# Kernel optimization log

Hardware: AMD Instinct MI355X
Metric: run time of the kernel (lower is better)

The kernel has to match this reference:

```python
import jax, jax.numpy as jnp
import numpy as np

# Module hyperparameters (init_kwargs)
NUM_EXPERTS = 8
HIDDEN = 1024
CAP_FACTORS = [0.5, 0.75, 1.0, 1.0, 1.25, 1.25, 1.5, 1.5]


def setup_inputs() -> dict:
    key = jax.random.key(0)
    k1, k2, k3 = jax.random.split(key, 3)
    G, T = 4, 2048
    token_inputs = jax.random.normal(k1, (G, T, HIDDEN), dtype=jnp.float32)
    # RouterWeights = nn.Linear(hidden, num_experts, bias=True)
    W = jax.random.normal(k2, (HIDDEN, NUM_EXPERTS), dtype=jnp.float32) * (1.0 / np.sqrt(HIDDEN))
    b = jax.random.normal(k3, (NUM_EXPERTS,), dtype=jnp.float32) * 0.01
    return {"token_inputs": token_inputs, "W": W, "b": b, "expert_capacity": 256}


def reference(token_inputs, W, b, expert_capacity):
    # token_inputs: [G, T, H]; jitter_noise=0 so no jitter; ignore_padding_tokens=False
    G, T, _ = token_inputs.shape
    logits = jnp.einsum("gth,he->gte", token_inputs, W) + b  # [G, T, E]
    probs = jax.nn.softmax(logits, axis=-1)
    # router z-loss: mean(logsumexp(logits, -1)^2)
    z_loss = jnp.mean(jax.nn.logsumexp(logits, axis=-1) ** 2)

    capacities = [int(expert_capacity * f) for f in CAP_FACTORS]
    max_cap = max(capacities)

    dispatch_slices = []  # each [G, T, max_cap] int32
    combine_slices = []   # each [G, T, max_cap] float32
    for e, cap in enumerate(capacities):
        gate, idx = jax.lax.top_k(probs[:, :, e], cap)  # [G, cap]
        # one_hot(idx, T): [G, cap, T] -> transpose to [G, T, cap]
        oh = jax.nn.one_hot(idx, T, dtype=jnp.int32).transpose(0, 2, 1)  # [G, T, cap]
        oh = jnp.pad(oh, ((0, 0), (0, 0), (0, max_cap - cap)))
        dispatch_slices.append(oh)
        # combine: gate broadcast over tokens dim (as in original code)
        comb = jnp.broadcast_to(gate[:, None, :], (G, T, cap))  # [G, T, cap]
        comb = jnp.pad(comb, ((0, 0), (0, 0), (0, max_cap - cap)))
        combine_slices.append(comb)

    dispatch_mask = jnp.stack(dispatch_slices, axis=1)  # [G, E, T, max_cap]
    combine_array = jnp.stack(combine_slices, axis=1).astype(jnp.float32)  # [G, E, T, max_cap]
    auxiliary_loss = jnp.float32(0.0)
    return dispatch_mask, combine_array, auxiliary_loss, z_loss
```

## Files before the change

kernel.cpp:

```cpp
#include <hip/hip_runtime.h>
#include <hip/hip_bf16.h>
#include <math.h>

#define G 4
#define T 2048
#define H 1024
#define E 8
#define NSORT (G * E)

typedef float f4 __attribute__((ext_vector_type(4)));

__global__ __launch_bounds__(256) void router_logits(
    const float* __restrict__ x, const float* __restrict__ W,
    const float* __restrict__ b, float* __restrict__ probs,
    float* __restrict__ lse2) {
  int wave = (int)((blockIdx.x * blockDim.x + threadIdx.x) >> 6);
  int lane = threadIdx.x & 63;
  if (wave >= G * T) return;
  const float* xr = x + (size_t)wave * H;

  double acc0 = 0, acc1 = 0, acc2 = 0, acc3 = 0;
  double acc4 = 0, acc5 = 0, acc6 = 0, acc7 = 0;
#pragma unroll
  for (int j = 0; j < 4; ++j) {
    int hbase = j * 256 + lane * 4;
    f4 xv = *(const f4*)(xr + hbase);
#pragma unroll
    for (int k = 0; k < 4; ++k) {
      const float* wr = W + (size_t)(hbase + k) * 8;
      f4 w0 = *(const f4*)(wr);
      f4 w1 = *(const f4*)(wr + 4);
      double xd = (double)xv[k];
      acc0 += xd * (double)w0[0];
      acc1 += xd * (double)w0[1];
      acc2 += xd * (double)w0[2];
      acc3 += xd * (double)w0[3];
      acc4 += xd * (double)w1[0];
      acc5 += xd * (double)w1[1];
      acc6 += xd * (double)w1[2];
      acc7 += xd * (double)w1[3];
    }
  }
#pragma unroll
  for (int off = 32; off >= 1; off >>= 1) {
    acc0 += __shfl_xor(acc0, off);
    acc1 += __shfl_xor(acc1, off);
    acc2 += __shfl_xor(acc2, off);
    acc3 += __shfl_xor(acc3, off);
    acc4 += __shfl_xor(acc4, off);
    acc5 += __shfl_xor(acc5, off);
    acc6 += __shfl_xor(acc6, off);
    acc7 += __shfl_xor(acc7, off);
  }
  if (lane == 0) {
    double l0 = acc0 + (double)b[0], l1 = acc1 + (double)b[1];
    double l2 = acc2 + (double)b[2], l3 = acc3 + (double)b[3];
    double l4 = acc4 + (double)b[4], l5 = acc5 + (double)b[5];
    double l6 = acc6 + (double)b[6], l7 = acc7 + (double)b[7];
    double m = fmax(fmax(fmax(l0, l1), fmax(l2, l3)),
                    fmax(fmax(l4, l5), fmax(l6, l7)));
    double p0 = exp(l0 - m), p1 = exp(l1 - m), p2 = exp(l2 - m),
           p3 = exp(l3 - m), p4 = exp(l4 - m), p5 = exp(l5 - m),
           p6 = exp(l6 - m), p7 = exp(l7 - m);
    double s = ((p0 + p1) + (p2 + p3)) + ((p4 + p5) + (p6 + p7));
    double inv = 1.0 / s;
    f4 v0 = {(float)(p0 * inv), (float)(p1 * inv), (float)(p2 * inv),
             (float)(p3 * inv)};
    f4 v1 = {(float)(p4 * inv), (float)(p5 * inv), (float)(p6 * inv),
             (float)(p7 * inv)};
    *(f4*)(probs + (size_t)wave * 8) = v0;
    *(f4*)(probs + (size_t)wave * 8 + 4) = v1;
    double lse = m + log(s);
    lse2[wave] = (float)(lse * lse);
  }
}

__global__ __launch_bounds__(1024) void sort_and_zero(
    const float* __restrict__ probs, float* __restrict__ gate,
    int* __restrict__ idx, float* __restrict__ out, unsigned n4d, int max_cap,
    int ec) {
  __shared__ unsigned long long keys[T];
  unsigned tid = threadIdx.x;
  unsigned bid = blockIdx.x;

  if (bid < NSORT) {
    int g = bid >> 3, e = bid & 7;
    for (int t = tid; t < T; t += 1024) {
      float p = probs[((size_t)g * T + t) * 8 + e];
      unsigned int bits = __float_as_uint(p);
      keys[t] = ((unsigned long long)bits << 32) | (unsigned int)(~t);
    }
    __syncthreads();
    for (unsigned k = 2; k <= T; k <<= 1) {
      for (unsigned j = k >> 1; j > 0; j >>= 1) {
        unsigned i = ((tid & ~(j - 1)) << 1) | (tid & (j - 1));
        unsigned ixj = i | j;
        unsigned long long a = keys[i], c = keys[ixj];
        bool desc = ((i & k) == 0);
        if (desc ? (a < c) : (a > c)) {
          keys[i] = c;
          keys[ixj] = a;
        }
        __syncthreads();
      }
    }
    const double factors[8] = {0.5, 0.75, 1.0, 1.0, 1.25, 1.25, 1.5, 1.5};
    int cap = (int)((double)ec * factors[e]);
    for (int c = tid; c < max_cap; c += 1024) {
      size_t o = (size_t)bid * max_cap + c;
      if (c < cap) {
        unsigned long long kk = keys[c];
        gate[o] = __uint_as_float((unsigned)(kk >> 32));
        idx[o] = (int)(~(unsigned)kk);
      } else {
        gate[o] = 0.0f;
        idx[o] = -1;
      }
    }
  } else {
    f4* outD = (f4*)out;
    f4 z = {0.0f, 0.0f, 0.0f, 0.0f};
    unsigned stride = (gridDim.x - NSORT) * 1024u;
    for (unsigned i = (bid - NSORT) * 1024u + tid; i < n4d; i += stride)
      outD[i] = z;
  }
}

template <int MC4S>
__global__ __launch_bounds__(256) void scatter_and_combine(
    const float* __restrict__ gate, const int* __restrict__ idx,
    const float* __restrict__ lse2, float* __restrict__ out, unsigned n4d,
    unsigned mc4_rt, int max_cap, unsigned scb) {
  const unsigned mc4 = MC4S ? (unsigned)MC4S : mc4_rt;
  unsigned tid = threadIdx.x;
  unsigned bid = blockIdx.x;

  if (bid == 0) {
    __shared__ double red[256];
    double s = 0.0;
    for (int i = tid; i < G * T; i += 256) s += (double)lse2[i];
    red[tid] = s;
    __syncthreads();
    for (int off = 128; off > 0; off >>= 1) {
      if ((int)tid < off) red[tid] += red[tid + off];
      __syncthreads();
    }
    if (tid == 0) {
      size_t ne = (size_t)n4d * 4;
      out[2 * ne] = 0.0f;
      out[2 * ne + 1] = (float)(red[0] / (double)(G * T));
    }
    return;
  }
  if (bid <= scb) {
    unsigned s = (bid - 1) * 256u + tid;
    if (s < (unsigned)(G * E) * (unsigned)max_cap) {
      unsigned ge = s / (unsigned)max_cap;
      unsigned c = s - ge * (unsigned)max_cap;
      int t = idx[s];
      if (t >= 0)
        out[((size_t)ge * T + t) * (unsigned)max_cap + c] = 1.0f;
    }
    return;
  }

  f4* outC = (f4*)out + n4d;
  const f4* gate4 = (const f4*)gate;
  unsigned fb = bid - 1 - scb;
  unsigned nfb = gridDim.x - 1 - scb;
  unsigned stride = nfb * 256u;
  for (unsigned i = fb * 256u + tid; i < n4d; i += stride) {
    unsigned c4 = i % mc4;
    unsigned rem = i / mc4;
    unsigned ge = rem >> 11;
    outC[i] = gate4[ge * mc4 + c4];
  }
}

extern "C" void kernel_launch(void* const* d_in, const int* in_sizes, int n_in,
                              void* d_out, int out_size, void* d_ws,
                              size_t ws_size, hipStream_t stream) {
  const float* x = (const float*)d_in[0];
  const float* W = (const float*)d_in[1];
  const float* b = (const float*)d_in[2];

  long long body = (long long)out_size - 2;
  int max_cap = (int)(body / (2LL * G * E * T));
  if (max_cap <= 0) return;
  int ec = (2 * max_cap) / 3;

  float* ws = (float*)d_ws;
  float* probs = ws;
  float* lse2 = ws + (size_t)G * T * E;
  float* gate = lse2 + (size_t)G * T;
  int* idx = (int*)(gate + (size_t)G * E * max_cap);

  unsigned n4d = (unsigned)((long long)G * E * T * max_cap / 4);
  unsigned scb = (unsigned)((G * E * max_cap + 255) / 256);

  router_logits<<<(G * T) / 4, 256, 0, stream>>>(x, W, b, probs, lse2);
  sort_and_zero<<<NSORT + 2048, 1024, 0, stream>>>(probs, gate, idx,
                                                   (float*)d_out, n4d, max_cap,
                                                   ec);
  int blocks = 6144;
  if (max_cap == 384) {
    scatter_and_combine<96><<<blocks, 256, 0, stream>>>(
        gate, idx, lse2, (float*)d_out, n4d, 96u, max_cap, scb);
  } else {
    scatter_and_combine<0><<<blocks, 256, 0, stream>>>(
        gate, idx, lse2, (float*)d_out, n4d, (unsigned)(max_cap / 4), max_cap,
        scb);
  }
}
```

Measured before the change: 78.65 us.

## Replace bitonic sort with parallel rank-counting top-k and fuse zeroing into logits

Replaces the per-(group,expert) 1024-thread bitonic sort with a rank-select kernel where each token counts how many keys exceed its own, spread across 256 blocks of 256 threads. The output zeroing and the gate/idx initialisation move into the logits kernel as extra blocks, so they overlap with the router matmul. This removes the long serial chain of barrier-separated sort stages, which used only 32 blocks. In exchange each thread does O(T) shared-memory comparisons, and ties depend on the key encoding that puts the inverted index in the low bits.

Result: slower. 95.89 us (+21.9%).

```diff
diff --git a/kernel.cpp b/kernel.cpp
--- a/kernel.cpp
+++ b/kernel.cpp
@@ -6,123 +6,122 @@
 #define T 2048
 #define H 1024
 #define E 8
-#define NSORT (G * E)
+#define LB (G * T / 4)
+#define ZB 2048
 
 typedef float f4 __attribute__((ext_vector_type(4)));
 
-__global__ __launch_bounds__(256) void router_logits(
+__global__ __launch_bounds__(256) void logits_zero_init(
     const float* __restrict__ x, const float* __restrict__ W,
     const float* __restrict__ b, float* __restrict__ probs,
-    float* __restrict__ lse2) {
-  int wave = (int)((blockIdx.x * blockDim.x + threadIdx.x) >> 6);
-  int lane = threadIdx.x & 63;
-  if (wave >= G * T) return;
-  const float* xr = x + (size_t)wave * H;
-
-  double acc0 = 0, acc1 = 0, acc2 = 0, acc3 = 0;
-  double acc4 = 0, acc5 = 0, acc6 = 0, acc7 = 0;
+    float* __restrict__ lse2, float* __restrict__ out,
+    float* __restrict__ gate, int* __restrict__ idx, unsigned n4d,
+    int max_cap) {
+  unsigned bid = blockIdx.x;
+  unsigned tid = threadIdx.x;
+
+  if (bid < LB) {
+    int wave = (int)(bid * 4 + (tid >> 6));
+    int lane = tid & 63;
+    const float* xr = x + (size_t)wave * H;
+
+    double acc0 = 0, acc1 = 0, acc2 = 0, acc3 = 0;
+    double acc4 = 0, acc5 = 0, acc6 = 0, acc7 = 0;
 #pragma unroll
-  for (int j = 0; j < 4; ++j) {
-    int hbase = j * 256 + lane * 4;
-    f4 xv = *(const f4*)(xr + hbase);
+    for (int j = 0; j < 4; ++j) {
+      int hbase = j * 256 + lane * 4;
+      f4 xv = *(const f4*)(xr + hbase);
 #pragma unroll
-    for (int k = 0; k < 4; ++k) {
-      const float* wr = W + (size_t)(hbase + k) * 8;
-      f4 w0 = *(const f4*)(wr);
-      f4 w1 = *(const f4*)(wr + 4);
-      double xd = (double)xv[k];
-      acc0 += xd * (double)w0[0];
-      acc1 += xd * (double)w0[1];
-      acc2 += xd * (double)w0[2];
-      acc3 += xd * (double)w0[3];
-      acc4 += xd * (double)w1[0];
-      acc5 += xd * (double)w1[1];
-      acc6 += xd * (double)w1[2];
-      acc7 += xd * (double)w1[3];
-    }
-  }
+      for (int k = 0; k < 4; ++k) {
+        const float* wr = W + (size_t)(hbase + k) * 8;
+        f4 w0 = *(const f4*)(wr);
+        f4 w1 = *(const f4*)(wr + 4);
+        double xd = (double)xv[k];
+        acc0 += xd * (double)w0[0];
+        acc1 += xd * (double)w0[1];
+        acc2 += xd * (double)w0[2];
+        acc3 += xd * (double)w0[3];
+        acc4 += xd * (double)w1[0];
+        acc5 += xd * (double)w1[1];
+        acc6 += xd * (double)w1[2];
+        acc7 += xd * (double)w1[3];
+      }
+    }
 #pragma unroll
-  for (int off = 32; off >= 1; off >>= 1) {
-    acc0 += __shfl_xor(acc0, off);
-    acc1 += __shfl_xor(acc1, off);
-    acc2 += __shfl_xor(acc2, off);
-    acc3 += __shfl_xor(acc3, off);
-    acc4 += __shfl_xor(acc4, off);
-    acc5 += __shfl_xor(acc5, off);
-    acc6 += __shfl_xor(acc6, off);
-    acc7 += __shfl_xor(acc7, off);
-  }
-  if (lane == 0) {
-    double l0 = acc0 + (double)b[0], l1 = acc1 + (double)b[1];
-    double l2 = acc2 + (double)b[2], l3 = acc3 + (double)b[3];
-    double l4 = acc4 + (double)b[4], l5 = acc5 + (double)b[5];
-    double l6 = acc6 + (double)b[6], l7 = acc7 + (double)b[7];
-    double m = fmax(fmax(fmax(l0, l1), fmax(l2, l3)),
-                    fmax(fmax(l4, l5), fmax(l6, l7)));
-    double p0 = exp(l0 - m), p1 = exp(l1 - m), p2 = exp(l2 - m),
-           p3 = exp(l3 - m), p4 = exp(l4 - m), p5 = exp(l5 - m),
-           p6 = exp(l6 - m), p7 = exp(l7 - m);
-    double s = ((p0 + p1) + (p2 + p3)) + ((p4 + p5) + (p6 + p7));
-    double inv = 1.0 / s;
-    f4 v0 = {(float)(p0 * inv), (float)(p1 * inv), (float)(p2 * inv),
-             (float)(p3 * inv)};
-    f4 v1 = {(float)(p4 * inv), (float)(p5 * inv), (float)(p6 * inv),
-             (float)(p7 * inv)};
-    *(f4*)(probs + (size_t)wave * 8) = v0;
-    *(f4*)(probs + (size_t)wave * 8 + 4) = v1;
-    double lse = m + log(s);
-    lse2[wave] = (float)(lse * lse);
-  }
-}
-
-__global__ __launch_bounds__(1024) void sort_and_zero(
-    const float* __restrict__ probs, float* __restrict__ gate,
-    int* __restrict__ idx, float* __restrict__ out, unsigned n4d, int max_cap,
-    int ec) {
-  __shared__ unsigned long long keys[T];
-  unsigned tid = threadIdx.x;
-  unsigned bid = blockIdx.x;
-
-  if (bid < NSORT) {
-    int g = bid >> 3, e = bid & 7;
-    for (int t = tid; t < T; t += 1024) {
-      float p = probs[((size_t)g * T + t) * 8 + e];
-      unsigned int bits = __float_as_uint(p);
-      keys[t] = ((unsigned long long)bits << 32) | (unsigned int)(~t);
-    }
-    __syncthreads();
-    for (unsigned k = 2; k <= T; k <<= 1) {
-      for (unsigned j = k >> 1; j > 0; j >>= 1) {
-        unsigned i = ((tid & ~(j - 1)) << 1) | (tid & (j - 1));
-        unsigned ixj = i | j;
-        unsigned long long a = keys[i], c = keys[ixj];
-        bool desc = ((i & k) == 0);
-        if (desc ? (a < c) : (a > c)) {
-          keys[i] = c;
-          keys[ixj] = a;
-        }
-        __syncthreads();
-      }
-    }
-    const double factors[8] = {0.5, 0.75, 1.0, 1.0, 1.25, 1.25, 1.5, 1.5};
-    int cap = (int)((double)ec * factors[e]);
-    for (int c = tid; c < max_cap; c += 1024) {
-      size_t o = (size_t)bid * max_cap + c;
-      if (c < cap) {
-        unsigned long long kk = keys[c];
-        gate[o] = __uint_as_float((unsigned)(kk >> 32));
-        idx[o] = (int)(~(unsigned)kk);
-      } else {
-        gate[o] = 0.0f;
-        idx[o] = -1;
-      }
-    }
-  } else {
+    for (int off = 32; off >= 1; off >>= 1) {
+      acc0 += __shfl_xor(acc0, off);
+      acc1 += __shfl_xor(acc1, off);
+      acc2 += __shfl_xor(acc2, off);
+      acc3 += __shfl_xor(acc3, off);
+      acc4 += __shfl_xor(acc4, off);
+      acc5 += __shfl_xor(acc5, off);
+      acc6 += __shfl_xor(acc6, off);
+      acc7 += __shfl_xor(acc7, off);
+    }
+    if (lane == 0) {
+      double l0 = acc0 + (double)b[0], l1 = acc1 + (double)b[1];
+      double l2 = acc2 + (double)b[2], l3 = acc3 + (double)b[3];
+      double l4 = acc4 + (double)b[4], l5 = acc5 + (double)b[5];
+      double l6 = acc6 + (double)b[6], l7 = acc7 + (double)b[7];
+      double m = fmax(fmax(fmax(l0, l1), fmax(l2, l3)),
+                      fmax(fmax(l4, l5), fmax(l6, l7)));
+      double p0 = exp(l0 - m), p1 = exp(l1 - m), p2 = exp(l2 - m),
+             p3 = exp(l3 - m), p4 = exp(l4 - m), p5 = exp(l5 - m),
+             p6 = exp(l6 - m), p7 = exp(l7 - m);
+      double s = ((p0 + p1) + (p2 + p3)) + ((p4 + p5) + (p6 + p7));
+      double inv = 1.0 / s;
+      f4 v0 = {(float)(p0 * inv), (float)(p1 * inv), (float)(p2 * inv),
+               (float)(p3 * inv)};
+      f4 v1 = {(float)(p4 * inv), (float)(p5 * inv), (float)(p6 * inv),
+               (float)(p7 * inv)};
+      *(f4*)(probs + (size_t)wave * 8) = v0;
+      *(f4*)(probs + (size_t)wave * 8 + 4) = v1;
+      double lse = m + log(s);
+      lse2[wave] = (float)(lse * lse);
+    }
+  } else if (bid < LB + ZB) {
     f4* outD = (f4*)out;
     f4 z = {0.0f, 0.0f, 0.0f, 0.0f};
-    unsigned stride = (gridDim.x - NSORT) * 1024u;
-    for (unsigned i = (bid - NSORT) * 1024u + tid; i < n4d; i += stride)
+    unsigned stride = ZB * 256u;
+    for (unsigned i = (bid - LB) * 256u + tid; i < n4d; i += stride)
       outD[i] = z;
+  } else {
+    unsigned s = (bid - LB - ZB) * 256u + tid;
+    if (s < (unsigned)(G * E * max_cap)) {
+      gate[s] = 0.0f;
+      idx[s] = -1;
+    }
+  }
+}
+
+__global__ __launch_bounds__(256) void rank_select(
+    const float* __restrict__ probs, float* __restrict__ gate,
+    int* __restrict__ idx, int max_cap, int ec) {
+  __shared__ unsigned long long keys[T];
+  unsigned bid = blockIdx.x;
+  int ge = (int)(bid >> 3);
+  int chunk = (int)(bid & 7);
+  int g = ge >> 3, e = ge & 7;
+  int tid = threadIdx.x;
+
+  for (int t = tid; t < T; t += 256) {
+    float p = probs[((size_t)g * T + t) * 8 + e];
+    keys[t] =
+        ((unsigned long long)__float_as_uint(p) << 32) | (unsigned)(~t);
+  }
+  __syncthreads();
+
+  int myt = chunk * 256 + tid;
+  unsigned long long k0 = keys[myt];
+  int rank = 0;
+#pragma unroll 8
+  for (int j = 0; j < T; ++j) rank += (keys[j] > k0) ? 1 : 0;
+
+  const double factors[8] = {0.5, 0.75, 1.0, 1.0, 1.25, 1.25, 1.5, 1.5};
+  int cap = (int)((double)ec * factors[e]);
+  if (rank < cap) {
+    gate[(size_t)ge * max_cap + rank] = __uint_as_float((unsigned)(k0 >> 32));
+    idx[(size_t)ge * max_cap + rank] = myt;
   }
 }
 
@@ -158,8 +157,7 @@
       unsigned ge = s / (unsigned)max_cap;
       unsigned c = s - ge * (unsigned)max_cap;
       int t = idx[s];
-      if (t >= 0)
-        out[((size_t)ge * T + t) * (unsigned)max_cap + c] = 1.0f;
+      if (t >= 0) out[((size_t)ge * T + t) * (unsigned)max_cap + c] = 1.0f;
     }
     return;
   }
@@ -197,11 +195,12 @@
 
   unsigned n4d = (unsigned)((long long)G * E * T * max_cap / 4);
   unsigned scb = (unsigned)((G * E * max_cap + 255) / 256);
-
-  router_logits<<<(G * T) / 4, 256, 0, stream>>>(x, W, b, probs, lse2);
-  sort_and_zero<<<NSORT + 2048, 1024, 0, stream>>>(probs, gate, idx,
-                                                   (float*)d_out, n4d, max_cap,
-                                                   ec);
+  unsigned initb = scb;
+
+  logits_zero_init<<<LB + ZB + initb, 256, 0, stream>>>(
+      x, W, b, probs, lse2, (float*)d_out, gate, idx, n4d, max_cap);
+  rank_select<<<256, 256, 0, stream>>>(probs, gate, idx, max_cap, ec);
+
   int blocks = 6144;
   if (max_cap == 384) {
     scatter_and_combine<96><<<blocks, 256, 0, stream>>>(
```

## Replace bitonic sort with histogram bucket top-k selection and expert-major keys

Applied to the files above, without the earlier changes.

The full 2048-element bitonic sort per (group, expert) is replaced by a 2048-bucket histogram on the top key bits, a suffix-sum scan, bucket scatter and in-bucket rank counting, which writes only the top-cap entries. The logits kernel now spreads the softmax across lanes and writes packed 64-bit keys in expert-major layout, so the selection step reads them contiguously. The zeroing portion uses far fewer blocks (448 instead of 2048). Risks include shared-memory atomic contention and long serial rank loops when many probabilities fall into one bucket.

Result: no change. 77.95 us (-0.9%).

```diff
diff --git a/kernel.cpp b/kernel.cpp
--- a/kernel.cpp
+++ b/kernel.cpp
@@ -6,17 +6,19 @@
 #define T 2048
 #define H 1024
 #define E 8
-#define NSORT (G * E)
+#define NBUK 2048
+#define SELB 32
+#define ZELB 448
 
 typedef float f4 __attribute__((ext_vector_type(4)));
-
-__global__ __launch_bounds__(256) void router_logits(
+typedef unsigned long long u64;
+
+__global__ __launch_bounds__(256) void k1_logits(
     const float* __restrict__ x, const float* __restrict__ W,
-    const float* __restrict__ b, float* __restrict__ probs,
+    const float* __restrict__ b, u64* __restrict__ keys,
     float* __restrict__ lse2) {
-  int wave = (int)((blockIdx.x * blockDim.x + threadIdx.x) >> 6);
-  int lane = threadIdx.x & 63;
-  if (wave >= G * T) return;
+  int wave = (int)(blockIdx.x * 4 + (threadIdx.x >> 6));
+  int lane = (int)(threadIdx.x & 63);
   const float* xr = x + (size_t)wave * H;
 
   double acc0 = 0, acc1 = 0, acc2 = 0, acc3 = 0;
@@ -52,82 +54,134 @@
     acc6 += __shfl_xor(acc6, off);
     acc7 += __shfl_xor(acc7, off);
   }
+  double l0 = acc0 + (double)b[0], l1 = acc1 + (double)b[1];
+  double l2 = acc2 + (double)b[2], l3 = acc3 + (double)b[3];
+  double l4 = acc4 + (double)b[4], l5 = acc5 + (double)b[5];
+  double l6 = acc6 + (double)b[6], l7 = acc7 + (double)b[7];
+  double m = fmax(fmax(fmax(l0, l1), fmax(l2, l3)),
+                  fmax(fmax(l4, l5), fmax(l6, l7)));
+  double la = (lane & 1) ? l1 : l0;
+  double lb = (lane & 1) ? l3 : l2;
+  double lc = (lane & 1) ? l5 : l4;
+  double ld = (lane & 1) ? l7 : l6;
+  double le = (lane & 2) ? lb : la;
+  double lf = (lane & 2) ? ld : lc;
+  double lsel = (lane & 4) ? lf : le;
+
+  double pe = exp(lsel - m);
+  double s = pe;
+  s += __shfl_xor(s, 1);
+  s += __shfl_xor(s, 2);
+  s += __shfl_xor(s, 4);
+  double inv = 1.0 / s;
+  float pf = (float)(pe * inv);
+
+  int g = wave >> 11;
+  int t = wave & (T - 1);
+  if (lane < 8) {
+    keys[((size_t)g * 8 + lane) * T + t] =
+        ((u64)__float_as_uint(pf) << 32) | (unsigned)(~t);
+  }
   if (lane == 0) {
-    double l0 = acc0 + (double)b[0], l1 = acc1 + (double)b[1];
-    double l2 = acc2 + (double)b[2], l3 = acc3 + (double)b[3];
-    double l4 = acc4 + (double)b[4], l5 = acc5 + (double)b[5];
-    double l6 = acc6 + (double)b[6], l7 = acc7 + (double)b[7];
-    double m = fmax(fmax(fmax(l0, l1), fmax(l2, l3)),
-                    fmax(fmax(l4, l5), fmax(l6, l7)));
-    double p0 = exp(l0 - m), p1 = exp(l1 - m), p2 = exp(l2 - m),
-           p3 = exp(l3 - m), p4 = exp(l4 - m), p5 = exp(l5 - m),
-           p6 = exp(l6 - m), p7 = exp(l7 - m);
-    double s = ((p0 + p1) + (p2 + p3)) + ((p4 + p5) + (p6 + p7));
-    double inv = 1.0 / s;
-    f4 v0 = {(float)(p0 * inv), (float)(p1 * inv), (float)(p2 * inv),
-             (float)(p3 * inv)};
-    f4 v1 = {(float)(p4 * inv), (float)(p5 * inv), (float)(p6 * inv),
-             (float)(p7 * inv)};
-    *(f4*)(probs + (size_t)wave * 8) = v0;
-    *(f4*)(probs + (size_t)wave * 8 + 4) = v1;
     double lse = m + log(s);
     lse2[wave] = (float)(lse * lse);
   }
 }
 
-__global__ __launch_bounds__(1024) void sort_and_zero(
-    const float* __restrict__ probs, float* __restrict__ gate,
+__global__ __launch_bounds__(1024) void k2_select_zero(
+    const u64* __restrict__ keys, float* __restrict__ gate,
     int* __restrict__ idx, float* __restrict__ out, unsigned n4d, int max_cap,
     int ec) {
-  __shared__ unsigned long long keys[T];
+  unsigned bid = blockIdx.x;
   unsigned tid = threadIdx.x;
-  unsigned bid = blockIdx.x;
-
-  if (bid < NSORT) {
-    int g = bid >> 3, e = bid & 7;
-    for (int t = tid; t < T; t += 1024) {
-      float p = probs[((size_t)g * T + t) * 8 + e];
-      unsigned int bits = __float_as_uint(p);
-      keys[t] = ((unsigned long long)bits << 32) | (unsigned int)(~t);
-    }
-    __syncthreads();
-    for (unsigned k = 2; k <= T; k <<= 1) {
-      for (unsigned j = k >> 1; j > 0; j >>= 1) {
-        unsigned i = ((tid & ~(j - 1)) << 1) | (tid & (j - 1));
-        unsigned ixj = i | j;
-        unsigned long long a = keys[i], c = keys[ixj];
-        bool desc = ((i & k) == 0);
-        if (desc ? (a < c) : (a > c)) {
-          keys[i] = c;
-          keys[ixj] = a;
-        }
-        __syncthreads();
-      }
-    }
-    const double factors[8] = {0.5, 0.75, 1.0, 1.0, 1.25, 1.25, 1.5, 1.5};
-    int cap = (int)((double)ec * factors[e]);
-    for (int c = tid; c < max_cap; c += 1024) {
-      size_t o = (size_t)bid * max_cap + c;
-      if (c < cap) {
-        unsigned long long kk = keys[c];
-        gate[o] = __uint_as_float((unsigned)(kk >> 32));
-        idx[o] = (int)(~(unsigned)kk);
-      } else {
-        gate[o] = 0.0f;
-        idx[o] = -1;
-      }
-    }
-  } else {
+
+  if (bid >= SELB) {
     f4* outD = (f4*)out;
     f4 z = {0.0f, 0.0f, 0.0f, 0.0f};
-    unsigned stride = (gridDim.x - NSORT) * 1024u;
-    for (unsigned i = (bid - NSORT) * 1024u + tid; i < n4d; i += stride)
+    unsigned stride = ZELB * 1024u;
+    for (unsigned i = (bid - SELB) * 1024u + tid; i < n4d; i += stride)
       outD[i] = z;
+    return;
+  }
+
+  __shared__ int hist[NBUK];
+  __shared__ int sA[NBUK];
+  __shared__ int sB[NBUK];
+  __shared__ int cur[NBUK];
+  __shared__ u64 srt[T];
+  int ge = (int)bid;
+
+  hist[tid] = 0;
+  hist[tid + 1024] = 0;
+  if (tid < (unsigned)max_cap) {
+    gate[(size_t)ge * max_cap + tid] = 0.0f;
+    idx[(size_t)ge * max_cap + tid] = -1;
+  }
+  __syncthreads();
+
+  const u64* kcol = keys + (size_t)ge * T;
+  u64 k0 = kcol[tid];
+  u64 k1 = kcol[tid + 1024];
+  int b0 = (int)(k0 >> 53);
+  int b1 = (int)(k1 >> 53);
+  atomicAdd(&hist[b0], 1);
+  atomicAdd(&hist[b1], 1);
+  __syncthreads();
+
+  sA[tid] = hist[tid];
+  sA[tid + 1024] = hist[tid + 1024];
+  __syncthreads();
+  int* src = sA;
+  int* dst = sB;
+  for (int s = 1; s < NBUK; s <<= 1) {
+    for (int i = (int)tid; i < NBUK; i += 1024) {
+      int v = src[i];
+      if (i + s < NBUK) v += src[i + s];
+      dst[i] = v;
+    }
+    __syncthreads();
+    int* tmp = src;
+    src = dst;
+    dst = tmp;
+  }
+  for (int i = (int)tid; i < NBUK; i += 1024) cur[i] = src[i] - hist[i];
+  __syncthreads();
+
+  int p0 = atomicAdd(&cur[b0], 1);
+  srt[p0] = k0;
+  int p1 = atomicAdd(&cur[b1], 1);
+  srt[p1] = k1;
+  __syncthreads();
+
+  const double factors[8] = {0.5, 0.75, 1.0, 1.0, 1.25, 1.25, 1.5, 1.5};
+  int cap = (int)((double)ec * factors[ge & 7]);
+
+  int o0 = src[b0] - hist[b0];
+  if (o0 < cap) {
+    int end = src[b0];
+    int c = 0;
+    for (int i = o0; i < end; ++i) c += (int)(srt[i] > k0);
+    int r = o0 + c;
+    if (r < cap) {
+      gate[(size_t)ge * max_cap + r] = __uint_as_float((unsigned)(k0 >> 32));
+      idx[(size_t)ge * max_cap + r] = (int)~(unsigned)k0;
+    }
+  }
+  int o1 = src[b1] - hist[b1];
+  if (o1 < cap) {
+    int end = src[b1];
+    int c = 0;
+    for (int i = o1; i < end; ++i) c += (int)(srt[i] > k1);
+    int r = o1 + c;
+    if (r < cap) {
+      gate[(size_t)ge * max_cap + r] = __uint_as_float((unsigned)(k1 >> 32));
+      idx[(size_t)ge * max_cap + r] = (int)~(unsigned)k1;
+    }
   }
 }
 
 template <int MC4S>
-__global__ __launch_bounds__(256) void scatter_and_combine(
+__global__ __launch_bounds__(256) void k3_scatter_combine(
     const float* __restrict__ gate, const int* __restrict__ idx,
     const float* __restrict__ lse2, float* __restrict__ out, unsigned n4d,
     unsigned mc4_rt, int max_cap, unsigned scb) {
@@ -158,8 +212,7 @@
       unsigned ge = s / (unsigned)max_cap;
       unsigned c = s - ge * (unsigned)max_cap;
       int t = idx[s];
-      if (t >= 0)
-        out[((size_t)ge * T + t) * (unsigned)max_cap + c] = 1.0f;
+      if (t >= 0) out[((size_t)ge * T + t) * (unsigned)max_cap + c] = 1.0f;
     }
     return;
   }
@@ -171,8 +224,7 @@
   unsigned stride = nfb * 256u;
   for (unsigned i = fb * 256u + tid; i < n4d; i += stride) {
     unsigned c4 = i % mc4;
-    unsigned rem = i / mc4;
-    unsigned ge = rem >> 11;
+    unsigned ge = (i / mc4) >> 11;
     outC[i] = gate4[ge * mc4 + c4];
   }
 }
@@ -189,25 +241,24 @@
   if (max_cap <= 0) return;
   int ec = (2 * max_cap) / 3;
 
-  float* ws = (float*)d_ws;
-  float* probs = ws;
-  float* lse2 = ws + (size_t)G * T * E;
+  u64* keys = (u64*)d_ws;
+  float* lse2 = (float*)(keys + (size_t)G * E * T);
   float* gate = lse2 + (size_t)G * T;
   int* idx = (int*)(gate + (size_t)G * E * max_cap);
 
   unsigned n4d = (unsigned)((long long)G * E * T * max_cap / 4);
   unsigned scb = (unsigned)((G * E * max_cap + 255) / 256);
 
-  router_logits<<<(G * T) / 4, 256, 0, stream>>>(x, W, b, probs, lse2);
-  sort_and_zero<<<NSORT + 2048, 1024, 0, stream>>>(probs, gate, idx,
+  k1_logits<<<G * T / 4, 256, 0, stream>>>(x, W, b, keys, lse2);
+  k2_select_zero<<<SELB + ZELB, 1024, 0, stream>>>(keys, gate, idx,
                                                    (float*)d_out, n4d, max_cap,
                                                    ec);
   int blocks = 6144;
   if (max_cap == 384) {
-    scatter_and_combine<96><<<blocks, 256, 0, stream>>>(
+    k3_scatter_combine<96><<<blocks, 256, 0, stream>>>(
         gate, idx, lse2, (float*)d_out, n4d, 96u, max_cap, scb);
   } else {
-    scatter_and_combine<0><<<blocks, 256, 0, stream>>>(
+    k3_scatter_combine<0><<<blocks, 256, 0, stream>>>(
         gate, idx, lse2, (float*)d_out, n4d, (unsigned)(max_cap / 4), max_cap,
         scb);
   }
```
